# Optimization experiments

Measured on AMD Instinct MI355X. Metric: run time of the kernel, lower is better.

The kernel has to match this reference:

```python
import jax, jax.numpy as jnp
import numpy as np
import math

B, L, H, U = 4, 4096, 1024, 1024


def setup_inputs() -> dict:
    key = jax.random.key(0)
    k_in, k_wi, k_bi, k_wo, k_bo, k_u = jax.random.split(key, 6)
    inputs = jax.random.normal(k_in, (B, L, H), dtype=jnp.float32)
    # Linear layers (torch Linear: y = x @ W.T + b), scaled like torch default init
    Wi = jax.random.normal(k_wi, (U, H), dtype=jnp.float32) / math.sqrt(H)
    bi = jax.random.normal(k_bi, (U,), dtype=jnp.float32) * 0.01
    Wo = jax.random.normal(k_wo, (H, U), dtype=jnp.float32) / math.sqrt(U)
    bo = jax.random.normal(k_bo, (H,), dtype=jnp.float32) * 0.01
    # LRU-style init of nu_log / gamma_log, exactly as in the torch __init__
    r_min, r_max = 0.9, 0.999
    u = jax.random.uniform(k_u, (U,), dtype=jnp.float32)
    nu_log = jnp.log(-0.5 * jnp.log(u * (r_max ** 2 - r_min ** 2) + r_min ** 2))
    gamma_log = jnp.log(jnp.sqrt(1.0 - jnp.exp(-jnp.exp(nu_log)) ** 2))
    params_log = jnp.stack([nu_log, gamma_log])  # [2, U]
    return {"inputs": inputs, "Wi": Wi, "bi": bi, "Wo": Wo, "bo": bo,
            "params_log": params_log}


def reference(inputs, Wi, bi, Wo, bo, params_log):
    # u = i_dense(inputs): [B, L, U]
    u = jnp.einsum('blh,uh->blu', inputs, Wi) + bi
    params = jnp.exp(params_log)
    nu, gamma = params[0], params[1]  # each [U]

    log2_L = int(np.ceil(np.log2(L)))
    pad_len = 2 ** log2_L - L
    x = jnp.pad(u, ((0, 0), (0, pad_len), (0, 0))) if pad_len else u
    Lp = 2 ** log2_L

    # Log-depth doubling parallel scan: h_t = exp(-nu) * h_{t-1} + u_t
    for i in range(1, log2_L + 1):
        l = 2 ** i
        x = x.reshape(B * Lp // l, l, U)
        x1, x2 = x[:, : l // 2], x[:, l // 2:]
        pos = jnp.arange(1, l // 2 + 1, dtype=jnp.float32)  # [l/2]
        lambs = jnp.exp(-pos[:, None] * nu)                  # [l/2, U]
        x2 = x2 + lambs * x1[:, -1:]
        x = jnp.concatenate([x1, x2], axis=1).reshape(B, Lp, U)

    x = x[:, :L] * gamma
    # o_dense: [B, L, H]
    return jnp.einsum('blu,hu->blh', x, Wo) + bo
```

## Files before the change

### kernel.cpp

```cpp
#include <hip/hip_runtime.h>

#define B_DIM 4
#define L_DIM 4096
#define H_DIM 1024
#define U_DIM 1024
#define M_DIM (B_DIM * L_DIM)
#define LC 64
#define NCH (L_DIM / LC)

using f32x4  = __attribute__((ext_vector_type(4))) float;
using bf16x8 = __attribute__((ext_vector_type(8))) __bf16;
using us8    = __attribute__((ext_vector_type(8))) unsigned short;
using u32x2  = __attribute__((ext_vector_type(2))) unsigned int;

__device__ inline unsigned short f32_to_bf16(float f) {
  unsigned int u = __float_as_uint(f);
  u += 0x7FFF + ((u >> 16) & 1);
  return (unsigned short)(u >> 16);
}
__device__ inline float bf16_to_f32(unsigned short v) {
  return __uint_as_float((unsigned int)v << 16);
}

__device__ inline void async_load16(const void* g, void* l) {
  __builtin_amdgcn_global_load_lds(
      (const __attribute__((address_space(1))) void*)g,
      (__attribute__((address_space(3))) void*)l, 16, 0, 0);
}

#define IN_ELEMS  (M_DIM * H_DIM)
#define WI_ELEMS  (U_DIM * H_DIM)
#define WO_ELEMS  (H_DIM * U_DIM)
#define CVT_TOTAL (IN_ELEMS + WI_ELEMS + WO_ELEMS)

__global__ __launch_bounds__(256) void cvt_all(
    const float* __restrict__ inp, const float* __restrict__ wi,
    const float* __restrict__ wo,
    unsigned short* __restrict__ inp_b, unsigned short* __restrict__ wi_b,
    unsigned short* __restrict__ wo_b)
{
  size_t e = ((size_t)blockIdx.x * 256 + threadIdx.x) * 8;
  if (e >= CVT_TOTAL) return;
  const float* src; unsigned short* dst; size_t off;
  if (e < IN_ELEMS)                 { src = inp; dst = inp_b; off = e; }
  else if (e < IN_ELEMS + WI_ELEMS) { src = wi;  dst = wi_b;  off = e - IN_ELEMS; }
  else                              { src = wo;  dst = wo_b;  off = e - IN_ELEMS - WI_ELEMS; }
  f32x4 a = *(const f32x4*)(src + off);
  f32x4 b = *(const f32x4*)(src + off + 4);
  us8 r;
  r[0] = f32_to_bf16(a.x); r[1] = f32_to_bf16(a.y);
  r[2] = f32_to_bf16(a.z); r[3] = f32_to_bf16(a.w);
  r[4] = f32_to_bf16(b.x); r[5] = f32_to_bf16(b.y);
  r[6] = f32_to_bf16(b.z); r[7] = f32_to_bf16(b.w);
  *(us8*)(dst + off) = r;
}

#define BM 256
#define BN 256
#define BK 64

template <typename OUT>
__global__ __launch_bounds__(512, 2) void gemm256(
    const unsigned short* __restrict__ A, const unsigned short* __restrict__ Bm,
    const float* __restrict__ bias, OUT* __restrict__ C,
    int M, int N, int K)
{
  __shared__ __attribute__((aligned(16))) char lds[131072];

  const int tid  = threadIdx.x;
  const int lane = tid & 63;
  const int wave = tid >> 6;
  const int wm   = wave >> 2;
  const int wn   = wave & 3;

  const int nby = M / BM;
  const int sby = nby >> 3;
  const int p   = blockIdx.x;
  const int xcd = p & 7;
  const int j   = p >> 3;
  const int by  = xcd * sby + (j % sby);
  const int bx  = j / sby;
  const int m0  = by * BM;
  const int n0  = bx * BN;

  const size_t rowb = (size_t)K * 2;
  const int NTk = K / BK;

  const int srow  = tid >> 3;
  const int scs16 = ((tid & 7) ^ (srow & 7)) << 4;
  const char* Ab = (const char*)A;
  const char* Bb = (const char*)Bm;

  auto stA = [&](int buf, int half, int kt) {
    const char* g = Ab + (size_t)(m0 + half * 128 + srow) * rowb + (size_t)kt * 128 + scs16;
    char* d = lds + buf * 65536 + half * 16384 + tid * 16;
    async_load16(g, d);
    async_load16(g + 64 * rowb, d + 8192);
  };
  auto stB = [&](int buf, int half, int kt) {
    const char* g = Bb + (size_t)(n0 + half * 128 + srow) * rowb + (size_t)kt * 128 + scs16;
    char* d = lds + buf * 65536 + 32768 + half * 16384 + tid * 16;
    async_load16(g, d);
    async_load16(g + 64 * rowb, d + 8192);
  };

  const int arow = wm * 128 + (lane & 15);
  const int brow = wn * 64  + (lane & 15);
  const int ch0  = (((lane >> 4)    ) ^ (lane & 7)) << 4;
  const int ch1  = (((lane >> 4) | 4) ^ (lane & 7)) << 4;

  f32x4 acc[8][4];
  #pragma unroll
  for (int i = 0; i < 8; ++i)
    #pragma unroll
    for (int q = 0; q < 4; ++q)
      acc[i][q] = {0.f, 0.f, 0.f, 0.f};

  stA(0, 0, 0); stA(0, 1, 0); stB(0, 0, 0); stB(0, 1, 0);
  stA(1, 0, 1); stA(1, 1, 1);
  asm volatile("s_waitcnt vmcnt(4)" ::: "memory");
  __builtin_amdgcn_sched_barrier(0);
  __builtin_amdgcn_s_barrier();

  for (int w = 0; w < NTk; ++w) {
    const int cur = w & 1;
    const char* pa = lds + cur * 65536 + arow * 128;
    const char* pb = lds + cur * 65536 + 32768 + brow * 128;
    bf16x8 af[8][2], bfr[4][2];

    #pragma unroll
    for (int mi = 0; mi < 4; ++mi) {
      af[mi][0] = *(const bf16x8*)(pa + mi * 2048 + ch0);
      af[mi][1] = *(const bf16x8*)(pa + mi * 2048 + ch1);
    }
    #pragma unroll
    for (int ni = 0; ni < 2; ++ni) {
      bfr[ni][0] = *(const bf16x8*)(pb + ni * 2048 + ch0);
      bfr[ni][1] = *(const bf16x8*)(pb + ni * 2048 + ch1);
    }
    if (w + 1 < NTk) stB(cur ^ 1, 0, w + 1);
    __builtin_amdgcn_s_barrier();
    asm volatile("s_waitcnt lgkmcnt(0)" ::: "memory");
    __builtin_amdgcn_sched_barrier(0);
    __builtin_amdgcn_s_setprio(1);
    #pragma unroll
    for (int mi = 0; mi < 4; ++mi)
      #pragma unroll
      for (int ni = 0; ni < 2; ++ni) {
        acc[mi][ni] = __builtin_amdgcn_mfma_f32_16x16x32_bf16(bfr[ni][0], af[mi][0], acc[mi][ni], 0, 0, 0);
        acc[mi][ni] = __builtin_amdgcn_mfma_f32_16x16x32_bf16(bfr[ni][1], af[mi][1], acc[mi][ni], 0, 0, 0);
      }
    __builtin_amdgcn_s_setprio(0);
    __builtin_amdgcn_s_barrier();

    #pragma unroll
    for (int mi = 4; mi < 8; ++mi) {
      af[mi][0] = *(const bf16x8*)(pa + mi * 2048 + ch0);
      af[mi][1] = *(const bf16x8*)(pa + mi * 2048 + ch1);
    }
    if (w + 1 < NTk) stB(cur ^ 1, 1, w + 1);
    __builtin_amdgcn_s_barrier();
    asm volatile("s_waitcnt lgkmcnt(0)" ::: "memory");
    __builtin_amdgcn_sched_barrier(0);
    __builtin_amdgcn_s_setprio(1);
    #pragma unroll
    for (int mi = 4; mi < 8; ++mi)
      #pragma unroll
      for (int ni = 0; ni < 2; ++ni) {
        acc[mi][ni] = __builtin_amdgcn_mfma_f32_16x16x32_bf16(bfr[ni][0], af[mi][0], acc[mi][ni], 0, 0, 0);
        acc[mi][ni] = __builtin_amdgcn_mfma_f32_16x16x32_bf16(bfr[ni][1], af[mi][1], acc[mi][ni], 0, 0, 0);
      }
    __builtin_amdgcn_s_setprio(0);
    __builtin_amdgcn_s_barrier();

    #pragma unroll
    for (int ni = 2; ni < 4; ++ni) {
      bfr[ni][0] = *(const bf16x8*)(pb + ni * 2048 + ch0);
      bfr[ni][1] = *(const bf16x8*)(pb + ni * 2048 + ch1);
    }
    if (w + 2 < NTk) stA(cur, 0, w + 2);
    __builtin_amdgcn_s_barrier();
    asm volatile("s_waitcnt lgkmcnt(0)" ::: "memory");
    __builtin_amdgcn_sched_barrier(0);
    __builtin_amdgcn_s_setprio(1);
    #pragma unroll
    for (int mi = 0; mi < 4; ++mi)
      #pragma unroll
      for (int ni = 2; ni < 4; ++ni) {
        acc[mi][ni] = __builtin_amdgcn_mfma_f32_16x16x32_bf16(bfr[ni][0], af[mi][0], acc[mi][ni], 0, 0, 0);
        acc[mi][ni] = __builtin_amdgcn_mfma_f32_16x16x32_bf16(bfr[ni][1], af[mi][1], acc[mi][ni], 0, 0, 0);
      }
    __builtin_amdgcn_s_setprio(0);
    __builtin_amdgcn_s_barrier();

    if (w + 2 < NTk) stA(cur, 1, w + 2);
    if (w < NTk - 2) asm volatile("s_waitcnt vmcnt(4)" ::: "memory");
    else             asm volatile("s_waitcnt vmcnt(0)" ::: "memory");
    __builtin_amdgcn_sched_barrier(0);
    __builtin_amdgcn_s_barrier();
    __builtin_amdgcn_s_setprio(1);
    #pragma unroll
    for (int mi = 4; mi < 8; ++mi)
      #pragma unroll
      for (int ni = 2; ni < 4; ++ni) {
        acc[mi][ni] = __builtin_amdgcn_mfma_f32_16x16x32_bf16(bfr[ni][0], af[mi][0], acc[mi][ni], 0, 0, 0);
        acc[mi][ni] = __builtin_amdgcn_mfma_f32_16x16x32_bf16(bfr[ni][1], af[mi][1], acc[mi][ni], 0, 0, 0);
      }
    __builtin_amdgcn_s_setprio(0);
    __builtin_amdgcn_s_barrier();
  }

  const int q4 = (lane >> 4) * 4;
  #pragma unroll
  for (int mi = 0; mi < 8; ++mi) {
    const int row = m0 + wm * 128 + mi * 16 + (lane & 15);
    #pragma unroll
    for (int ni = 0; ni < 4; ++ni) {
      const int ncol = n0 + wn * 64 + ni * 16 + q4;
      const f32x4 bv = *(const f32x4*)(bias + ncol);
      f32x4 v = acc[mi][ni];
      v.x += bv.x; v.y += bv.y; v.z += bv.z; v.w += bv.w;
      if constexpr (sizeof(OUT) == 2) {
        u32x2 pk;
        pk.x = ((unsigned)f32_to_bf16(v.y) << 16) | (unsigned)f32_to_bf16(v.x);
        pk.y = ((unsigned)f32_to_bf16(v.w) << 16) | (unsigned)f32_to_bf16(v.z);
        *(u32x2*)((unsigned short*)C + (size_t)row * N + ncol) = pk;
      } else {
        *(f32x4*)((float*)C + (size_t)row * N + ncol) = v;
      }
    }
  }
}

__global__ __launch_bounds__(256) void scan_carry(
    const unsigned short* __restrict__ u, const float* __restrict__ params_log,
    float* __restrict__ carry)
{
  int uu = blockIdx.x * 256 + threadIdx.x;
  int c  = blockIdx.y;
  int b  = blockIdx.z;
  float l = expf(-expf(params_log[uu]));
  const unsigned short* p = u + (size_t)(b * L_DIM + c * LC) * U_DIM + uu;
  float s = 0.f;
  #pragma unroll 8
  for (int j = 0; j < LC; ++j)
    s = fmaf(s, l, bf16_to_f32(p[(size_t)j * U_DIM]));
  carry[((size_t)b * NCH + c) * U_DIM + uu] = s;
}

__global__ __launch_bounds__(256) void scan_prefix(
    const float* __restrict__ carry, const float* __restrict__ params_log,
    float* __restrict__ prefix)
{
  int t  = blockIdx.x * 256 + threadIdx.x;
  int b  = t >> 10;
  int uu = t & (U_DIM - 1);
  float lp = expf(-expf(params_log[uu]) * (float)LC);
  const float* cp = carry  + (size_t)b * NCH * U_DIM + uu;
  float*       pp = prefix + (size_t)b * NCH * U_DIM + uu;
  float vals[NCH];
  #pragma unroll
  for (int c = 0; c < NCH; ++c)
    vals[c] = cp[(size_t)c * U_DIM];
  float s = 0.f;
  #pragma unroll
  for (int c = 0; c < NCH; ++c) {
    pp[(size_t)c * U_DIM] = s;
    s = fmaf(s, lp, vals[c]);
  }
}

__global__ __launch_bounds__(256) void scan_apply(
    const unsigned short* __restrict__ u, const float* __restrict__ params_log,
    const float* __restrict__ prefix, unsigned short* __restrict__ x_b)
{
  int uu = blockIdx.x * 256 + threadIdx.x;
  int c  = blockIdx.y;
  int b  = blockIdx.z;
  float l = expf(-expf(params_log[uu]));
  float g = expf(params_log[U_DIM + uu]);
  float s = prefix[((size_t)b * NCH + c) * U_DIM + uu];
  const unsigned short* p = u + (size_t)(b * L_DIM + c * LC) * U_DIM + uu;
  unsigned short* q = x_b + (size_t)(b * L_DIM + c * LC) * U_DIM + uu;
  #pragma unroll 8
  for (int j = 0; j < LC; ++j) {
    s = fmaf(s, l, bf16_to_f32(p[(size_t)j * U_DIM]));
    q[(size_t)j * U_DIM] = f32_to_bf16(s * g);
  }
}

extern "C" void kernel_launch(void* const* d_in, const int* in_sizes, int n_in,
                              void* d_out, int out_size, void* d_ws, size_t ws_size,
                              hipStream_t stream)
{
  const float* inputs     = (const float*)d_in[0];
  const float* Wi         = (const float*)d_in[1];
  const float* bi         = (const float*)d_in[2];
  const float* Wo         = (const float*)d_in[3];
  const float* bo         = (const float*)d_in[4];
  const float* params_log = (const float*)d_in[5];
  float* out = (float*)d_out;

  char* ws = (char*)d_ws;
  unsigned short* u_b    = (unsigned short*)(ws);
  unsigned short* x_b    = (unsigned short*)(ws + (32u << 20));
  unsigned short* in_b   = (unsigned short*)(ws + (64u << 20));
  unsigned short* wi_b   = (unsigned short*)(ws + (96u << 20));
  unsigned short* wo_b   = (unsigned short*)(ws + (98u << 20));
  float*          carry  = (float*)(ws + (100u << 20));
  float*          prefix = (float*)(ws + (101u << 20));

  cvt_all<<<dim3((CVT_TOTAL / 8 + 255) / 256), 256, 0, stream>>>(
      inputs, Wi, Wo, in_b, wi_b, wo_b);

  gemm256<unsigned short><<<dim3((M_DIM / BM) * (U_DIM / BN)), 512, 0, stream>>>(
      in_b, wi_b, bi, u_b, M_DIM, U_DIM, H_DIM);

  scan_carry <<<dim3(U_DIM / 256, NCH, B_DIM), 256, 0, stream>>>(u_b, params_log, carry);
  scan_prefix<<<dim3(B_DIM * U_DIM / 256),     256, 0, stream>>>(carry, params_log, prefix);
  scan_apply <<<dim3(U_DIM / 256, NCH, B_DIM), 256, 0, stream>>>(u_b, params_log, prefix, x_b);

  gemm256<float><<<dim3((M_DIM / BM) * (H_DIM / BN)), 512, 0, stream>>>(
      x_b, wo_b, bo, out, M_DIM, H_DIM, U_DIM);
}
```

Before: 231.9 us.

## Drop GEMM phase barriers, merge A-tile stores, and wave-parallelize chunk prefix scan

Removes the trailing s_barrier after each MFMA phase in the GEMM main loop and issues both halves of the next A tile store together before the vmcnt wait. This cuts synchronisation overhead between MFMA clusters, at the risk of LDS hazards if the remaining barriers do not fully order reads of the buffer being overwritten. It also rewrites scan_prefix so that each 64-lane wave runs a log-step shuffle scan over the 64 chunks of one (batch, unit) column instead of one thread doing a serial loop, which adds parallelism to a small latency-bound kernel.

```diff
diff --git a/kernel.cpp b/kernel.cpp
--- a/kernel.cpp
+++ b/kernel.cpp
@@ -151,7 +151,6 @@
         acc[mi][ni] = __builtin_amdgcn_mfma_f32_16x16x32_bf16(bfr[ni][1], af[mi][1], acc[mi][ni], 0, 0, 0);
       }
     __builtin_amdgcn_s_setprio(0);
-    __builtin_amdgcn_s_barrier();
 
     #pragma unroll
     for (int mi = 4; mi < 8; ++mi) {
@@ -171,14 +170,12 @@
         acc[mi][ni] = __builtin_amdgcn_mfma_f32_16x16x32_bf16(bfr[ni][1], af[mi][1], acc[mi][ni], 0, 0, 0);
       }
     __builtin_amdgcn_s_setprio(0);
-    __builtin_amdgcn_s_barrier();
 
     #pragma unroll
     for (int ni = 2; ni < 4; ++ni) {
       bfr[ni][0] = *(const bf16x8*)(pb + ni * 2048 + ch0);
       bfr[ni][1] = *(const bf16x8*)(pb + ni * 2048 + ch1);
     }
-    if (w + 2 < NTk) stA(cur, 0, w + 2);
     __builtin_amdgcn_s_barrier();
     asm volatile("s_waitcnt lgkmcnt(0)" ::: "memory");
     __builtin_amdgcn_sched_barrier(0);
@@ -191,9 +188,8 @@
         acc[mi][ni] = __builtin_amdgcn_mfma_f32_16x16x32_bf16(bfr[ni][1], af[mi][1], acc[mi][ni], 0, 0, 0);
       }
     __builtin_amdgcn_s_setprio(0);
-    __builtin_amdgcn_s_barrier();
-
-    if (w + 2 < NTk) stA(cur, 1, w + 2);
+
+    if (w + 2 < NTk) { stA(cur, 0, w + 2); stA(cur, 1, w + 2); }
     if (w < NTk - 2) asm volatile("s_waitcnt vmcnt(4)" ::: "memory");
     else             asm volatile("s_waitcnt vmcnt(0)" ::: "memory");
     __builtin_amdgcn_sched_barrier(0);
@@ -207,7 +203,6 @@
         acc[mi][ni] = __builtin_amdgcn_mfma_f32_16x16x32_bf16(bfr[ni][1], af[mi][1], acc[mi][ni], 0, 0, 0);
       }
     __builtin_amdgcn_s_setprio(0);
-    __builtin_amdgcn_s_barrier();
   }
 
   const int q4 = (lane >> 4) * 4;
@@ -252,22 +247,23 @@
     const float* __restrict__ carry, const float* __restrict__ params_log,
     float* __restrict__ prefix)
 {
-  int t  = blockIdx.x * 256 + threadIdx.x;
-  int b  = t >> 10;
-  int uu = t & (U_DIM - 1);
+  int wid  = (blockIdx.x * 256 + threadIdx.x) >> 6;
+  int lane = threadIdx.x & 63;
+  int b  = wid >> 10;
+  int uu = wid & (U_DIM - 1);
   float lp = expf(-expf(params_log[uu]) * (float)LC);
-  const float* cp = carry  + (size_t)b * NCH * U_DIM + uu;
-  float*       pp = prefix + (size_t)b * NCH * U_DIM + uu;
-  float vals[NCH];
+  const float* cp = carry + (size_t)b * NCH * U_DIM + uu;
+  float s = cp[(size_t)lane * U_DIM];
+  float a = lp;
   #pragma unroll
-  for (int c = 0; c < NCH; ++c)
-    vals[c] = cp[(size_t)c * U_DIM];
-  float s = 0.f;
-  #pragma unroll
-  for (int c = 0; c < NCH; ++c) {
-    pp[(size_t)c * U_DIM] = s;
-    s = fmaf(s, lp, vals[c]);
+  for (int d = 1; d < 64; d <<= 1) {
+    float s_up = __shfl_up(s, d, 64);
+    float a_up = __shfl_up(a, d, 64);
+    if (lane >= d) { s = fmaf(a, s_up, s); a *= a_up; }
   }
+  float ex = __shfl_up(s, 1, 64);
+  if (lane == 0) ex = 0.f;
+  prefix[((size_t)b * NCH + lane) * U_DIM + uu] = ex;
 }
 
 __global__ __launch_bounds__(256) void scan_apply(
@@ -317,7 +313,7 @@
       in_b, wi_b, bi, u_b, M_DIM, U_DIM, H_DIM);
 
   scan_carry <<<dim3(U_DIM / 256, NCH, B_DIM), 256, 0, stream>>>(u_b, params_log, carry);
-  scan_prefix<<<dim3(B_DIM * U_DIM / 256),     256, 0, stream>>>(carry, params_log, prefix);
+  scan_prefix<<<dim3(B_DIM * U_DIM * 64 / 256), 256, 0, stream>>>(carry, params_log, prefix);
   scan_apply <<<dim3(U_DIM / 256, NCH, B_DIM), 256, 0, stream>>>(u_b, params_log, prefix, x_b);
 
   gemm256<float><<<dim3((M_DIM / BM) * (H_DIM / BN)), 512, 0, stream>>>(
```

After: 227.3 us (median of 3 runs). 2.0% less time.
